# Performance work log

Measured on AMD Instinct MI355X. Metric: run time of the kernel, lower is better.

## Reference

```python
import jax, jax.numpy as jnp
from jax import lax
import numpy as np

PH, PW = 5, 5      # patch_shape; forced to 5x5 by the (batch, F, 27) reshape in AdaptiveConv
F = 32             # adaptive conv output channels
SCALE = 4          # super-resolution upscale factor


def conv2d(x, w, b, padding):
    # x: NCHW, w: OIHW
    y = lax.conv_general_dilated(x, w, (1, 1), padding,
                                 dimension_numbers=('NCHW', 'OIHW', 'NCHW'))
    return y + b[None, :, None, None]


def space_to_batch(x):
    # non-overlapping PHxPW tiles, order (batch, tile_row, tile_col) like the torch loops
    B, C, H, W = x.shape
    hn, wn = H // PH, W // PW
    p = x.reshape(B, C, hn, PH, wn, PW).transpose(0, 2, 4, 1, 3, 5)
    return p.reshape(B * hn * wn, C, PH, PW), (B, hn, wn)


def batch_to_space(p, meta):
    B, hn, wn = meta
    C = p.shape[1]
    out = p.reshape(B, hn, wn, C, PH, PW).transpose(0, 3, 1, 4, 2, 5)
    return out.reshape(B, C, hn * PH, wn * PW)


def unfold3(x):
    # torch F.unfold(x, 3, padding=1): (N, C*9, L) channel-major (c, kh, kw); return (N, L, C*9)
    N, C, H, W = x.shape
    xp = jnp.pad(x, ((0, 0), (0, 0), (1, 1), (1, 1)))
    cols = jnp.stack([xp[:, :, i:i + H, j:j + W]
                      for i in range(3) for j in range(3)], axis=2)  # (N, C, 9, H, W)
    return cols.reshape(N, C * 9, H * W).transpose(0, 2, 1)


def pixel_shuffle(x, r):
    B, Cr2, H, W = x.shape
    C = Cr2 // (r * r)
    return (x.reshape(B, C, r, r, H, W)
             .transpose(0, 1, 4, 2, 5, 3)
             .reshape(B, C, H * r, W * r))


def setup_inputs() -> dict:
    key = jax.random.key(0)
    ks = jax.random.split(key, 13)
    rn = lambda k, shape, s=0.05: jax.random.normal(k, shape, jnp.float32) * s
    return dict(
        x=jax.random.normal(ks[0], (2, 3, 360, 640), jnp.float32),
        w_feat=rn(ks[1], (256, 3, 3, 3)),        b_feat=rn(ks[2], (256,)),
        w_kern=rn(ks[3], (27 * F, 256, 3, 3)),   b_kern=rn(ks[4], (27 * F,)),
        w_badp=rn(ks[5], (F, 256, 3, 3)),        b_badp=rn(ks[6], (F,)),
        w1=rn(ks[7], (128, F, 5, 5)),            b1=rn(ks[8], (128,)),
        w2=rn(ks[9], (32, 128, 3, 3)),           b2=rn(ks[10], (32,)),
        w3=rn(ks[11], (3 * SCALE * SCALE, 32, 3, 3)), b3=rn(ks[12], (3 * SCALE * SCALE,)),
    )


def reference(x, w_feat, b_feat, w_kern, b_kern, w_badp, b_badp,
              w1, b1, w2, b2, w3, b3):
    patches, meta = space_to_batch(x)                        # (N, 3, 5, 5)
    N = patches.shape[0]
    # AdaptiveConv: per-patch dynamic 3x3 conv
    feat = jax.nn.relu(conv2d(patches, w_feat, b_feat, 'VALID'))   # (N, 256, 3, 3)
    kern = conv2d(feat, w_kern, b_kern, 'VALID')                   # (N, 27F, 1, 1)
    kern = kern.reshape(N, F, 27).transpose(0, 2, 1)               # (N, 27, F)
    xu = unfold3(patches)                                          # (N, 25, 27)
    out = jnp.einsum('nlk,nkf->nlf', xu, kern)                     # (N, 25, F)
    out = out.transpose(0, 2, 1).reshape(N, F, PH, PW)
    bias = conv2d(feat, w_badp, b_badp, 'VALID')                   # (N, F, 1, 1)
    out = jax.nn.relu(out + bias)
    sp = batch_to_space(out, meta)                                 # (B, F, H, W)
    # RegularConv stack
    h = jax.nn.relu(conv2d(sp, w1, b1, 'SAME'))
    h = jax.nn.relu(conv2d(h, w2, b2, 'SAME'))
    h = conv2d(h, w3, b3, 'SAME')                                  # (B, 3*r*r, H, W)
    return pixel_shuffle(h, SCALE)                                 # (B, 3, H*r, W*r)
```

## Files before the change

kernel.cpp:

```cpp
#include <hip/hip_runtime.h>
#include <stdint.h>

typedef unsigned short ushort;
typedef __bf16 bf16x8 __attribute__((ext_vector_type(8)));
typedef float f32x4 __attribute__((ext_vector_type(4)));
typedef ushort ushort8 __attribute__((ext_vector_type(8)));
typedef ushort us4 __attribute__((ext_vector_type(4)));

__device__ __forceinline__ float bf2f(ushort u) {
  union { unsigned int i; float f; } v; v.i = ((unsigned int)u) << 16; return v.f;
}
__device__ __forceinline__ ushort f2bf(float f) {
  union { float f; unsigned int i; } v; v.f = f;
  unsigned int r = v.i + 0x7fffu + ((v.i >> 16) & 1u);
  return (ushort)(r >> 16);
}
__device__ __forceinline__ void glds16(const ushort* g, ushort* l) {
  __builtin_amdgcn_global_load_lds(
      (const __attribute__((address_space(1))) void*)g,
      (__attribute__((address_space(3))) void*)l, 16, 0, 0);
}

__global__ __launch_bounds__(256) void pack_kernel(
    const float* __restrict__ w_kern, const float* __restrict__ b_kern,
    const float* __restrict__ w_badp, const float* __restrict__ b_badp,
    ushort* __restrict__ Bt, float* __restrict__ bias896) {
  int idx = blockIdx.x * 256 + threadIdx.x;
  const int total = 896 * 2304;
  if (idx < total) {
    int o = idx / 2304, k = idx - o * 2304;
    int c = k & 255, pos = k >> 8;
    float v = (o < 864) ? w_kern[(o * 256 + c) * 9 + pos]
                        : w_badp[((o - 864) * 256 + c) * 9 + pos];
    Bt[idx] = f2bf(v);
  } else if (idx < total + 896) {
    int o = idx - total;
    bias896[o] = (o < 864) ? b_kern[o] : b_badp[o - 864];
  }
}

__global__ __launch_bounds__(256) void pack2_kernel(
    const float* __restrict__ w1, const float* __restrict__ w2,
    const float* __restrict__ w3, ushort* __restrict__ wp1,
    ushort* __restrict__ wp2, ushort* __restrict__ wp3) {
  int idx = blockIdx.x * 256 + threadIdx.x;
  if (idx < 102400) {
    int t = idx >> 12, rm = idx & 4095, o = rm >> 5, c = rm & 31;
    wp1[idx] = f2bf(w1[(o * 32 + c) * 25 + t]);
  } else if (idx < 102400 + 36864) {
    int j = idx - 102400;
    int t = j >> 12, rm = j & 4095, o = rm >> 7, c = rm & 127;
    wp2[j] = f2bf(w2[(o * 128 + c) * 9 + t]);
  } else if (idx < 102400 + 36864 + 13824) {
    int j = idx - 139264;
    int t = j / 1536, rm = j - t * 1536, o = rm >> 5, c = rm & 31;
    wp3[j] = f2bf(w3[(o * 32 + c) * 9 + t]);
  }
}

__global__ __launch_bounds__(256) void feat_kernel(
    const float* __restrict__ x, const float* __restrict__ w_feat,
    const float* __restrict__ b_feat, ushort* __restrict__ feat) {
  __shared__ float xp[4][3][5][5];
  const int t = threadIdx.x;
  const int n0 = blockIdx.x * 4;
  for (int e = t; e < 300; e += 256) {
    int p = e / 75, rem = e - p * 75;
    int ci = rem / 25, r = rem - ci * 25, i = r / 5, j = r - i * 5;
    int n = n0 + p;
    int b = n / 9216, ph = (n >> 7) % 72, pw = n & 127;
    xp[p][ci][i][j] = x[((b * 3 + ci) * 360 + ph * 5 + i) * 640 + pw * 5 + j];
  }
  float wf[27];
#pragma unroll
  for (int m = 0; m < 27; ++m) wf[m] = w_feat[t * 27 + m];
  const float bv = b_feat[t];
  __syncthreads();
  for (int p = 0; p < 4; ++p) {
    ushort* dst = feat + (size_t)(n0 + p) * 2304 + t;
#pragma unroll
    for (int pi = 0; pi < 3; ++pi)
#pragma unroll
      for (int pj = 0; pj < 3; ++pj) {
        float acc = bv;
#pragma unroll
        for (int ci = 0; ci < 3; ++ci)
#pragma unroll
          for (int ki = 0; ki < 3; ++ki)
#pragma unroll
            for (int kj = 0; kj < 3; ++kj)
              acc = fmaf(xp[p][ci][pi + ki][pj + kj], wf[ci * 9 + ki * 3 + kj], acc);
        dst[(pi * 3 + pj) * 256] = f2bf(fmaxf(acc, 0.f));
      }
  }
}

__global__ __launch_bounds__(256) void gemm_kernel(
    const ushort* __restrict__ A, const ushort* __restrict__ Bt,
    const float* __restrict__ bias, ushort* __restrict__ C) {
  const int K = 2304, N = 896;
  __shared__ __align__(16) ushort lA[2][128 * 32];
  __shared__ __align__(16) ushort lB[2][128 * 32];
  const int bid = blockIdx.x;
  const int xcd = bid & 7, j = bid >> 3;
  const int mblk = xcd * 18 + j / 7, nblk = j % 7;
  const int m0 = mblk * 128, n0 = nblk * 128;
  const int t = threadIdx.x;
  const int lane = t & 63, wave = t >> 6;
  const int wm = wave >> 1, wn = wave & 1;
  const int lp = lane & 15, lk = lane >> 4;
  f32x4 acc[4][4] = {};
  const int srow = t >> 2;
  const int sslot = (t & 3) ^ ((srow >> 1) & 3);
  const ushort* gA = A + (size_t)(m0 + srow) * K + sslot * 8;
  const ushort* gB = Bt + (size_t)(n0 + srow) * K + sslot * 8;
  const int swz = lk ^ ((lp >> 1) & 3);
  const int aoff = (wm * 64 + lp) * 32 + swz * 8;
  const int boff = (wn * 64 + lp) * 32 + swz * 8;

#define GSTAGE(buf, kt)                                   \
  do {                                                    \
    glds16(gA + (kt), &lA[buf][wave * 512]);              \
    glds16(gA + 64 * K + (kt), &lA[buf][2048 + wave * 512]); \
    glds16(gB + (kt), &lB[buf][wave * 512]);              \
    glds16(gB + 64 * K + (kt), &lB[buf][2048 + wave * 512]); \
  } while (0)

#define GCOMP(buf)                                                            \
  do {                                                                        \
    bf16x8 af[4], bfr[4];                                                     \
    _Pragma("unroll") for (int mi = 0; mi < 4; ++mi)                          \
        af[mi] = __builtin_bit_cast(bf16x8,                                   \
            *(const ushort8*)(&lA[buf][aoff + mi * 512]));                    \
    _Pragma("unroll") for (int ni = 0; ni < 4; ++ni)                          \
        bfr[ni] = __builtin_bit_cast(bf16x8,                                  \
            *(const ushort8*)(&lB[buf][boff + ni * 512]));                    \
    _Pragma("unroll") for (int mi = 0; mi < 4; ++mi)                          \
        _Pragma("unroll") for (int ni = 0; ni < 4; ++ni)                      \
            acc[mi][ni] = __builtin_amdgcn_mfma_f32_16x16x32_bf16(            \
                af[mi], bfr[ni], acc[mi][ni], 0, 0, 0);                       \
  } while (0)

  GSTAGE(0, 0);
  __syncthreads();
#pragma unroll 1
  for (int kt = 0; kt < K; kt += 64) {
    GSTAGE(1, kt + 32);
    GCOMP(0);
    __syncthreads();
    if (kt + 64 < K) GSTAGE(0, kt + 64);
    GCOMP(1);
    __syncthreads();
  }
#undef GSTAGE
#undef GCOMP

#pragma unroll
  for (int ni = 0; ni < 4; ++ni) {
    int col = n0 + wn * 64 + ni * 16 + lp;
    float bv = bias[col];
#pragma unroll
    for (int mi = 0; mi < 4; ++mi) {
      int row0 = m0 + wm * 64 + mi * 16 + lk * 4;
#pragma unroll
      for (int r = 0; r < 4; ++r)
        C[(size_t)(row0 + r) * N + col] = f2bf(acc[mi][ni][r] + bv);
    }
  }
}

__global__ __launch_bounds__(256) void apply_kernel(
    const float* __restrict__ x, const ushort* __restrict__ kernbias,
    ushort* __restrict__ sp) {
  __shared__ float xp[8][3][7][7];
  __shared__ ushort outl[8][32][25];
  const int t = threadIdx.x;
  const int n0 = blockIdx.x * 8;
  const int b = n0 / 9216, ph = (n0 >> 7) % 72, pw0 = n0 & 127;
  for (int e = t; e < 8 * 3 * 49; e += 256) ((float*)xp)[e] = 0.f;
  __syncthreads();
  for (int e = t; e < 600; e += 256) {
    int p = e / 75, rem = e - p * 75;
    int ci = rem / 25, r = rem - ci * 25, i = r / 5, j = r - i * 5;
    xp[p][ci][i + 1][j + 1] = x[((b * 3 + ci) * 360 + ph * 5 + i) * 640 + (pw0 + p) * 5 + j];
  }
  __syncthreads();
  const int p = t >> 5, f = t & 31;
  const int n = n0 + p;
  float kk[27];
#pragma unroll
  for (int k = 0; k < 27; ++k) kk[k] = bf2f(kernbias[(size_t)n * 896 + f * 27 + k]);
  const float bv = bf2f(kernbias[(size_t)n * 896 + 864 + f]);
  for (int l = 0; l < 25; ++l) {
    int li = l / 5, lj = l - li * 5;
    float s = bv;
#pragma unroll
    for (int k = 0; k < 27; ++k) {
      int ci = k / 9, rm = k - ci * 9, ki = rm / 3, kj = rm - ki * 3;
      s = fmaf(xp[p][ci][li + ki][lj + kj], kk[k], s);
    }
    outl[p][f][l] = f2bf(fmaxf(s, 0.f));
  }
  __syncthreads();
  for (int e = t; e < 6400; e += 256) {
    int f2 = e & 31;
    int idx = e >> 5;
    int i = idx / 40, c40 = idx - i * 40;
    int pp = c40 / 5, j = c40 - pp * 5;
    sp[(((size_t)b * 360 + ph * 5 + i) * 640 + pw0 * 5 + c40) * 32 + f2] = outl[pp][f2][i * 5 + j];
  }
}

__global__ __launch_bounds__(512, 4) void conv1_kernel(
    const ushort* __restrict__ sp, const ushort* __restrict__ wp1,
    const float* __restrict__ b1, ushort* __restrict__ h1) {
  __shared__ ushort8 lin[8 * 4 * 69];
  __shared__ ushort8 wbuf[2][1024];
  const int t = threadIdx.x;
  const int lane = t & 63, wave = t >> 6;
  const int wh = wave >> 1, wn = wave & 1;
  const int lp = lane & 15, lk = lane >> 4;
  const int w0 = blockIdx.x * 64, h0 = blockIdx.y * 4, b = blockIdx.z;
  for (int u = t; u < 8 * 4 * 68; u += 512) {
    int c8 = u & 3, rest = u >> 2;
    int wx = rest % 68, r = rest / 68;
    int gh = h0 - 2 + r, gw = w0 - 2 + wx;
    ushort8 v = {};
    if ((unsigned)gh < 360u && (unsigned)gw < 640u)
      v = *(const ushort8*)(sp + (((size_t)b * 360 + gh) * 640 + gw) * 32 + c8 * 8);
    lin[(r * 4 + c8) * 69 + wx] = v;
  }
  ushort* wd0 = (ushort*)&wbuf[0][wave * 64];
  ushort* wd1 = (ushort*)&wbuf[1][wave * 64];
  glds16(wp1 + t * 8, wd0);
  __syncthreads();

  f32x4 acc[4][4] = {};
#pragma unroll
  for (int tp = 0; tp < 25; ++tp) {
    if (tp < 24)
      glds16(wp1 + (tp + 1) * 4096 + t * 8, ((tp + 1) & 1) ? wd1 : wd0);
    const int ki = tp / 5, kj = tp % 5;
    const ushort8* wb8 = wbuf[tp & 1];
    bf16x8 W[4], Af[4];
#pragma unroll
    for (int nf = 0; nf < 4; ++nf)
      W[nf] = __builtin_bit_cast(bf16x8, wb8[(wn * 64 + nf * 16 + lp) * 4 + lk]);
    const int ab = (wh + ki) * 276 + lk * 69 + lp + kj;
#pragma unroll
    for (int mf = 0; mf < 4; ++mf)
      Af[mf] = __builtin_bit_cast(bf16x8, lin[ab + mf * 16]);
#pragma unroll
    for (int mf = 0; mf < 4; ++mf)
#pragma unroll
      for (int nf = 0; nf < 4; ++nf)
        acc[mf][nf] = __builtin_amdgcn_mfma_f32_16x16x32_bf16(W[nf], Af[mf], acc[mf][nf], 0, 0, 0);
    if (tp < 24) __syncthreads();
  }

  const int h = h0 + wh;
#pragma unroll
  for (int nf = 0; nf < 4; ++nf) {
    const int oc0 = wn * 64 + nf * 16 + lk * 4;
    f32x4 bv = *(const f32x4*)(b1 + oc0);
#pragma unroll
    for (int mf = 0; mf < 4; ++mf) {
      const int w = w0 + mf * 16 + lp;
      us4 pk;
#pragma unroll
      for (int r = 0; r < 4; ++r) pk[r] = f2bf(fmaxf(acc[mf][nf][r] + bv[r], 0.f));
      *(us4*)(&h1[(((size_t)b * 360 + h) * 640 + w) * 128 + oc0]) = pk;
    }
  }
}

__device__ __forceinline__ void c2_load(ushort8* stg, const ushort* __restrict__ h1,
                                        int t, int b, int h0, int w0, int cb) {
#pragma unroll
  for (int j = 0; j < 7; ++j) {
    int u = t + j * 256;
    ushort8 v = {};
    if (u < 1584) {
      int r = u / 264, rem = u - r * 264;
      int c8 = rem / 66, wx = rem - c8 * 66;
      int gh = h0 - 1 + r, gw = w0 - 1 + wx;
      if ((unsigned)gh < 360u && (unsigned)gw < 640u)
        v = *(const ushort8*)(h1 + (((size_t)b * 360 + gh) * 640 + gw) * 128 + cb * 32 + c8 * 8);
    }
    stg[j] = v;
  }
}
__device__ __forceinline__ void c2_write(const ushort8* stg, ushort8* buf, int t) {
#pragma unroll
  for (int j = 0; j < 7; ++j) {
    int u = t + j * 256;
    if (u < 1584) {
      int r = u / 264, rem = u - r * 264;
      int c8 = rem / 66, wx = rem - c8 * 66;
      buf[c8 * 414 + r * 69 + wx] = stg[j];
    }
  }
}
__device__ __forceinline__ void c2_compute(const ushort8* buf, const ushort* __restrict__ wp2,
                                           int cb, int wave, int lp, int lk, f32x4 acc[4][2]) {
#pragma unroll
  for (int ki = 0; ki < 3; ++ki) {
    const int rb = lk * 414 + (wave + ki) * 69;
#pragma unroll
    for (int kj = 0; kj < 3; ++kj) {
      const int tap = ki * 3 + kj;
      bf16x8 bfr[2];
#pragma unroll
      for (int nf = 0; nf < 2; ++nf) {
        ushort8 tmp = *(const ushort8*)(wp2 + tap * 4096 + nf * 2048 + lp * 128 + cb * 32 + lk * 8);
        bfr[nf] = __builtin_bit_cast(bf16x8, tmp);
      }
      bf16x8 afr[4];
#pragma unroll
      for (int mf = 0; mf < 4; ++mf)
        afr[mf] = __builtin_bit_cast(bf16x8, buf[rb + lp + mf * 16 + kj]);
#pragma unroll
      for (int mf = 0; mf < 4; ++mf)
#pragma unroll
        for (int nf = 0; nf < 2; ++nf)
          acc[mf][nf] = __builtin_amdgcn_mfma_f32_16x16x32_bf16(bfr[nf], afr[mf], acc[mf][nf], 0, 0, 0);
    }
  }
}

__global__ __launch_bounds__(256) void conv2_kernel(
    const ushort* __restrict__ h1, const ushort* __restrict__ wp2,
    const float* __restrict__ b2, ushort* __restrict__ h2) {
  __shared__ ushort8 lin[2][4 * 414];
  const int t = threadIdx.x;
  const int lane = t & 63, wave = t >> 6;
  const int lp = lane & 15, lk = lane >> 4;
  const int w0 = blockIdx.x * 64, h0 = blockIdx.y * 4, b = blockIdx.z;
  f32x4 acc[4][2] = {};
  ushort8 stg[7];
  c2_load(stg, h1, t, b, h0, w0, 0);
#pragma unroll
  for (int it = 0; it < 5; ++it) {
    __syncthreads();
    if (it < 4) c2_write(stg, lin[it & 1], t);
    if (it < 3) c2_load(stg, h1, t, b, h0, w0, it + 1);
    if (it >= 1) c2_compute(lin[(it - 1) & 1], wp2, it - 1, wave, lp, lk, acc);
  }
  const int h = h0 + wave;
#pragma unroll
  for (int nf = 0; nf < 2; ++nf) {
    const int oc0 = nf * 16 + lk * 4;
    f32x4 bv = *(const f32x4*)(b2 + oc0);
#pragma unroll
    for (int mf = 0; mf < 4; ++mf) {
      const int w = w0 + mf * 16 + lp;
      us4 pk;
#pragma unroll
      for (int r = 0; r < 4; ++r) pk[r] = f2bf(fmaxf(acc[mf][nf][r] + bv[r], 0.f));
      *(us4*)(&h2[(((size_t)b * 360 + h) * 640 + w) * 32 + oc0]) = pk;
    }
  }
}

__global__ __launch_bounds__(256) void conv3_kernel(
    const ushort* __restrict__ h2, const ushort* __restrict__ wp3,
    const float* __restrict__ b3, float* __restrict__ out) {
  __shared__ ushort8 lin[4 * 4 * 67];
  const int t = threadIdx.x;
  const int lane = t & 63, wave = t >> 6;
  const int wh = wave & 1, wm = wave >> 1;
  const int lp = lane & 15, lk = lane >> 4;
  const int w0 = blockIdx.x * 64, h0 = blockIdx.y * 2, b = blockIdx.z;
  for (int u = t; u < 4 * 4 * 66; u += 256) {
    int c8 = u & 3, rest = u >> 2;
    int wx = rest % 66, r = rest / 66;
    int gh = h0 - 1 + r, gw = w0 - 1 + wx;
    ushort8 v = {};
    if (gh >= 0 && gh < 360 && gw >= 0 && gw < 640)
      v = *(const ushort8*)(h2 + (((size_t)b * 360 + gh) * 640 + gw) * 32 + c8 * 8);
    lin[(r * 4 + c8) * 67 + wx] = v;
  }
  __syncthreads();
  f32x4 acc[2][3] = {};
  const int abase = lk * 67 + wm * 32 + lp;
  const ushort* wbase = wp3 + lp * 32 + lk * 8;
#pragma unroll
  for (int ki = 0; ki < 3; ++ki) {
#pragma unroll
    for (int kj = 0; kj < 3; ++kj) {
      const int tap = ki * 3 + kj;
      bf16x8 bfr[3];
#pragma unroll
      for (int nf = 0; nf < 3; ++nf) {
        ushort8 tmp = *(const ushort8*)(wbase + (size_t)tap * 1536 + nf * 512);
        bfr[nf] = __builtin_bit_cast(bf16x8, tmp);
      }
      bf16x8 afr[2];
#pragma unroll
      for (int mf = 0; mf < 2; ++mf)
        afr[mf] = __builtin_bit_cast(bf16x8, lin[(wh + ki) * 268 + abase + mf * 16 + kj]);
#pragma unroll
      for (int mf = 0; mf < 2; ++mf)
#pragma unroll
        for (int nf = 0; nf < 3; ++nf)
          acc[mf][nf] = __builtin_amdgcn_mfma_f32_16x16x32_bf16(bfr[nf], afr[mf], acc[mf][nf], 0, 0, 0);
    }
  }
  const int h = h0 + wh;
#pragma unroll
  for (int nf = 0; nf < 3; ++nf) {
    f32x4 bv = *(const f32x4*)(b3 + nf * 16 + lk * 4);
#pragma unroll
    for (int mf = 0; mf < 2; ++mf) {
      const int w = w0 + wm * 32 + mf * 16 + lp;
      f32x4 o;
#pragma unroll
      for (int r = 0; r < 4; ++r) o[r] = acc[mf][nf][r] + bv[r];
      *(f32x4*)(&out[(((size_t)b * 3 + nf) * 1440 + h * 4 + lk) * 2560 + (size_t)w * 4]) = o;
    }
  }
}

extern "C" void kernel_launch(void* const* d_in, const int* in_sizes, int n_in,
                              void* d_out, int out_size, void* d_ws, size_t ws_size,
                              hipStream_t stream) {
  const float* x      = (const float*)d_in[0];
  const float* w_feat = (const float*)d_in[1];
  const float* b_feat = (const float*)d_in[2];
  const float* w_kern = (const float*)d_in[3];
  const float* b_kern = (const float*)d_in[4];
  const float* w_badp = (const float*)d_in[5];
  const float* b_badp = (const float*)d_in[6];
  const float* w1 = (const float*)d_in[7];
  const float* b1 = (const float*)d_in[8];
  const float* w2 = (const float*)d_in[9];
  const float* b2 = (const float*)d_in[10];
  const float* w3 = (const float*)d_in[11];
  const float* b3 = (const float*)d_in[12];

  char* ws = (char*)d_ws;
  ushort* feat     = (ushort*)(ws);
  ushort* h1       = (ushort*)(ws);
  ushort* kernbias = (ushort*)(ws + 117964800);
  ushort* h2       = (ushort*)(ws + 117964800);
  ushort* wp1      = (ushort*)(ws + 147456000);
  ushort* wp2      = (ushort*)(ws + 147660800);
  ushort* wp3      = (ushort*)(ws + 147734528);
  ushort* sp       = (ushort*)(ws + 150994944);
  ushort* Bt       = (ushort*)(ws + 180486144);
  float*  bias896  = (float*)(ws + 184614912);

  pack_kernel<<<(896 * 2304 + 896 + 255) / 256, 256, 0, stream>>>(
      w_kern, b_kern, w_badp, b_badp, Bt, bias896);
  feat_kernel<<<4608, 256, 0, stream>>>(x, w_feat, b_feat, feat);
  gemm_kernel<<<1008, 256, 0, stream>>>(feat, Bt, bias896, kernbias);
  apply_kernel<<<2304, 256, 0, stream>>>(x, kernbias, sp);
  pack2_kernel<<<598, 256, 0, stream>>>(w1, w2, w3, wp1, wp2, wp3);
  conv1_kernel<<<dim3(10, 90, 2), 512, 0, stream>>>(sp, wp1, b1, h1);
  conv2_kernel<<<dim3(10, 90, 2), 256, 0, stream>>>(h1, wp2, b2, h2);
  conv3_kernel<<<dim3(10, 180, 2), 256, 0, stream>>>(h2, wp3, b3, (float*)d_out);
}
```

Measured before the change: 466.2 us.

## Deepen LDS prefetch pipelines in GEMM and conv1 with vmcnt-gated barriers

The GEMM moves from double to triple buffering of its A and B tiles in LDS. Each step waits with s_waitcnt vmcnt plus a raw barrier, so only the oldest stage has to land and two stages stay in flight. Conv1 gets the same treatment with four rotating weight buffers and three taps prefetched ahead, which removes the end-of-iteration __syncthreads. It also XOR-swizzles the weight layout in LDS to cut bank conflicts. The aim is to hide global load latency better, at the cost of extra LDS use in the GEMM, some redundant clamped tail loads, and hand-tuned waitcnt logic that is fragile if the load count per stage changes.

```diff
diff --git a/kernel.cpp b/kernel.cpp
--- a/kernel.cpp
+++ b/kernel.cpp
@@ -20,6 +20,13 @@
       (const __attribute__((address_space(1))) void*)g,
       (__attribute__((address_space(3))) void*)l, 16, 0, 0);
 }
+
+#define VMB(N)                                                  \
+  do {                                                          \
+    asm volatile("s_waitcnt vmcnt(" #N ")" ::: "memory");       \
+    __builtin_amdgcn_s_barrier();                               \
+    __builtin_amdgcn_sched_barrier(0);                          \
+  } while (0)
 
 __global__ __launch_bounds__(256) void pack_kernel(
     const float* __restrict__ w_kern, const float* __restrict__ b_kern,
@@ -99,8 +106,8 @@
     const ushort* __restrict__ A, const ushort* __restrict__ Bt,
     const float* __restrict__ bias, ushort* __restrict__ C) {
   const int K = 2304, N = 896;
-  __shared__ __align__(16) ushort lA[2][128 * 32];
-  __shared__ __align__(16) ushort lB[2][128 * 32];
+  __shared__ __align__(16) ushort lA[3][4096];
+  __shared__ __align__(16) ushort lB[3][4096];
   const int bid = blockIdx.x;
   const int xcd = bid & 7, j = bid >> 3;
   const int mblk = xcd * 18 + j / 7, nblk = j % 7;
@@ -118,12 +125,13 @@
   const int aoff = (wm * 64 + lp) * 32 + swz * 8;
   const int boff = (wn * 64 + lp) * 32 + swz * 8;
 
-#define GSTAGE(buf, kt)                                   \
-  do {                                                    \
-    glds16(gA + (kt), &lA[buf][wave * 512]);              \
-    glds16(gA + 64 * K + (kt), &lA[buf][2048 + wave * 512]); \
-    glds16(gB + (kt), &lB[buf][wave * 512]);              \
-    glds16(gB + 64 * K + (kt), &lB[buf][2048 + wave * 512]); \
+#define KT(x) ((x) < 2304 ? (x) : 2272)
+#define GSTAGE(buf, kt)                                       \
+  do {                                                        \
+    glds16(gA + (kt), &lA[buf][wave * 512]);                  \
+    glds16(gA + 64 * K + (kt), &lA[buf][2048 + wave * 512]);  \
+    glds16(gB + (kt), &lB[buf][wave * 512]);                  \
+    glds16(gB + 64 * K + (kt), &lB[buf][2048 + wave * 512]);  \
   } while (0)
 
 #define GCOMP(buf)                                                            \
@@ -142,18 +150,16 @@
   } while (0)
 
   GSTAGE(0, 0);
-  __syncthreads();
+  GSTAGE(1, 32);
 #pragma unroll 1
-  for (int kt = 0; kt < K; kt += 64) {
-    GSTAGE(1, kt + 32);
-    GCOMP(0);
-    __syncthreads();
-    if (kt + 64 < K) GSTAGE(0, kt + 64);
-    GCOMP(1);
-    __syncthreads();
+  for (int i = 0; i < 72; i += 3) {
+    VMB(4); GSTAGE(2, KT((i + 2) * 32)); GCOMP(0);
+    VMB(4); GSTAGE(0, KT((i + 3) * 32)); GCOMP(1);
+    VMB(4); GSTAGE(1, KT((i + 4) * 32)); GCOMP(2);
   }
 #undef GSTAGE
 #undef GCOMP
+#undef KT
 
 #pragma unroll
   for (int ni = 0; ni < 4; ++ni) {
@@ -215,12 +221,17 @@
     const ushort* __restrict__ sp, const ushort* __restrict__ wp1,
     const float* __restrict__ b1, ushort* __restrict__ h1) {
   __shared__ ushort8 lin[8 * 4 * 69];
-  __shared__ ushort8 wbuf[2][1024];
+  __shared__ ushort8 wbuf[4][512];
   const int t = threadIdx.x;
   const int lane = t & 63, wave = t >> 6;
   const int wh = wave >> 1, wn = wave & 1;
   const int lp = lane & 15, lk = lane >> 4;
   const int w0 = blockIdx.x * 64, h0 = blockIdx.y * 4, b = blockIdx.z;
+  const int srcoff = (t >> 2) * 32 + (((t & 3) ^ ((t >> 3) & 3)) * 8);
+#define WSTAGE(bf, tap) glds16(wp1 + (tap) * 4096 + srcoff, (ushort*)&wbuf[bf][wave * 64])
+  WSTAGE(0, 0);
+  WSTAGE(1, 1);
+  WSTAGE(2, 2);
   for (int u = t; u < 8 * 4 * 68; u += 512) {
     int c8 = u & 3, rest = u >> 2;
     int wx = rest % 68, r = rest / 68;
@@ -230,22 +241,23 @@
       v = *(const ushort8*)(sp + (((size_t)b * 360 + gh) * 640 + gw) * 32 + c8 * 8);
     lin[(r * 4 + c8) * 69 + wx] = v;
   }
-  ushort* wd0 = (ushort*)&wbuf[0][wave * 64];
-  ushort* wd1 = (ushort*)&wbuf[1][wave * 64];
-  glds16(wp1 + t * 8, wd0);
   __syncthreads();
 
   f32x4 acc[4][4] = {};
+  const int wswz = lk ^ ((lp >> 1) & 3);
 #pragma unroll
   for (int tp = 0; tp < 25; ++tp) {
-    if (tp < 24)
-      glds16(wp1 + (tp + 1) * 4096 + t * 8, ((tp + 1) & 1) ? wd1 : wd0);
+    VMB(2);
+    {
+      const int tn = (tp + 3 < 25) ? tp + 3 : 24;
+      WSTAGE((tp + 3) & 3, tn);
+    }
     const int ki = tp / 5, kj = tp % 5;
-    const ushort8* wb8 = wbuf[tp & 1];
+    const ushort8* wb8 = wbuf[tp & 3];
     bf16x8 W[4], Af[4];
 #pragma unroll
     for (int nf = 0; nf < 4; ++nf)
-      W[nf] = __builtin_bit_cast(bf16x8, wb8[(wn * 64 + nf * 16 + lp) * 4 + lk]);
+      W[nf] = __builtin_bit_cast(bf16x8, wb8[(wn * 64 + nf * 16 + lp) * 4 + wswz]);
     const int ab = (wh + ki) * 276 + lk * 69 + lp + kj;
 #pragma unroll
     for (int mf = 0; mf < 4; ++mf)
@@ -255,8 +267,8 @@
 #pragma unroll
       for (int nf = 0; nf < 4; ++nf)
         acc[mf][nf] = __builtin_amdgcn_mfma_f32_16x16x32_bf16(W[nf], Af[mf], acc[mf][nf], 0, 0, 0);
-    if (tp < 24) __syncthreads();
-  }
+  }
+#undef WSTAGE
 
   const int h = h0 + wh;
 #pragma unroll
```

Result: faster. 448.2 us (-3.8%).
